# Optimization experiments

Hardware: AMD Instinct MI355X
Metric: run time of the kernel (lower is better)

The kernel has to match this reference:

```python
import jax, jax.numpy as jnp
from jax import lax
import numpy as np

# Model hyperparameters (match init_kwargs)
NUM_STEPS = 6
N_ETYPES = 8
D_IN = 128
D_OUT = 128
B, N, E = 32, 1024, 262144  # graphs, nodes per graph, total edges


def setup_inputs() -> dict:
    key = jax.random.key(0)
    ks = jax.random.split(key, 24)
    s = 0.05  # param scale for numeric stability over 6 GRU steps
    inp = {
        "h": jax.random.normal(ks[0], (B, N, D_IN), jnp.float32),
        "src": jax.random.randint(ks[1], (E,), 0, B * N, jnp.int32),
        "dst": jax.random.randint(ks[2], (E,), 0, B * N, jnp.int32),
        "etype": jax.random.randint(ks[3], (E,), 0, N_ETYPES, jnp.int32),
        "W_msg": jax.random.normal(ks[4], (N_ETYPES, D_OUT, D_OUT), jnp.float32) * s,
        "b_msg": jax.random.normal(ks[5], (N_ETYPES, D_OUT), jnp.float32) * s,
        "w_ih": jax.random.normal(ks[6], (3 * D_OUT, D_OUT), jnp.float32) * s,
        "w_hh": jax.random.normal(ks[7], (3 * D_OUT, D_OUT), jnp.float32) * s,
        "b_ih": jax.random.normal(ks[8], (3 * D_OUT,), jnp.float32) * s,
        "b_hh": jax.random.normal(ks[9], (3 * D_OUT,), jnp.float32) * s,
        "conv1_w": jax.random.normal(ks[10], (D_OUT, D_OUT, 3), jnp.float32) * s,
        "conv1_b": jax.random.normal(ks[11], (D_OUT,), jnp.float32) * s,
        "conv2_w": jax.random.normal(ks[12], (D_OUT, D_OUT, 1), jnp.float32) * s,
        "conv2_b": jax.random.normal(ks[13], (D_OUT,), jnp.float32) * s,
        "cc1_w": jax.random.normal(ks[14], (D_IN + D_OUT, D_IN + D_OUT, 3), jnp.float32) * s,
        "cc1_b": jax.random.normal(ks[15], (D_IN + D_OUT,), jnp.float32) * s,
        "cc2_w": jax.random.normal(ks[16], (D_IN + D_OUT, D_IN + D_OUT, 1), jnp.float32) * s,
        "cc2_b": jax.random.normal(ks[17], (D_IN + D_OUT,), jnp.float32) * s,
        "mlp_y_w": jax.random.normal(ks[18], (1, D_OUT), jnp.float32) * s,
        "mlp_y_b": jax.random.normal(ks[19], (1,), jnp.float32) * s,
        "mlp_z_w": jax.random.normal(ks[20], (1, D_IN + D_OUT), jnp.float32) * s,
        "mlp_z_b": jax.random.normal(ks[21], (1,), jnp.float32) * s,
    }
    return inp


def _conv1d(x, w, b):
    # x: [B, C_in, L], w: [C_out, C_in, K]
    y = lax.conv_general_dilated(x, w, (1,), "VALID",
                                 dimension_numbers=("NCW", "OIW", "NCW"))
    return y + b[None, :, None]


def _maxpool1d(x, k, stride):
    return lax.reduce_window(x, -jnp.inf, lax.max,
                             (1, 1, k), (1, 1, stride), "VALID")


def _ggnn(h0, src, dst, etype, W_msg, b_msg, w_ih, w_hh, b_ih, b_hh):
    # h0: [BN, D_OUT] (in_feats == out_feats so no zero-padding needed)
    n_nodes = h0.shape[0]

    def step(h, _):
        # transform each node by every etype weight: [BN, T, O]
        t = jnp.einsum("nd,tod->nto", h, W_msg) + b_msg
        m = t[src, etype]                                   # [E, O] gather
        a = jax.ops.segment_sum(m, dst, num_segments=n_nodes)  # scatter-add
        # torch.nn.GRUCell(a, h)
        gi = a @ w_ih.T + b_ih
        gh = h @ w_hh.T + b_hh
        i_r, i_z, i_n = jnp.split(gi, 3, axis=-1)
        h_r, h_z, h_n = jnp.split(gh, 3, axis=-1)
        r = jax.nn.sigmoid(i_r + h_r)
        z = jax.nn.sigmoid(i_z + h_z)
        n = jnp.tanh(i_n + r * h_n)
        return (1.0 - z) * n + z * h, None

    h_final, _ = lax.scan(step, h0, None, length=NUM_STEPS)
    return h_final


def reference(h, src, dst, etype, W_msg, b_msg, w_ih, w_hh, b_ih, b_hh,
              conv1_w, conv1_b, conv2_w, conv2_b, cc1_w, cc1_b, cc2_w, cc2_b,
              mlp_y_w, mlp_y_b, mlp_z_w, mlp_z_b):
    b, n, d = h.shape
    x = h.reshape(b * n, d)
    h_next = _ggnn(x, src, dst, etype, W_msg, b_msg, w_ih, w_hh, b_ih, b_hh)
    h_i = h_next.reshape(b, n, -1)                   # [B, N, O]
    c_i = jnp.concatenate([h_i, h], axis=-1)          # [B, N, O+D]

    Y_1 = _maxpool1d(jax.nn.relu(_conv1d(h_i.transpose(0, 2, 1), conv1_w, conv1_b)), 3, 2)
    Y_2 = _maxpool1d(jax.nn.relu(_conv1d(Y_1, conv2_w, conv2_b)), 2, 2).transpose(0, 2, 1)
    Z_1 = _maxpool1d(jax.nn.relu(_conv1d(c_i.transpose(0, 2, 1), cc1_w, cc1_b)), 3, 2)
    Z_2 = _maxpool1d(jax.nn.relu(_conv1d(Z_1, cc2_w, cc2_b)), 2, 2).transpose(0, 2, 1)

    before_avg = (Y_2 @ mlp_y_w.T + mlp_y_b) * (Z_2 @ mlp_z_w.T + mlp_z_b)  # [B, L, 1]
    avg = before_avg.mean(axis=1)                     # [B, 1]
    return jax.nn.sigmoid(avg).squeeze(-1)            # [B]
```

## Files before the change

### kernel.cpp

```cpp
#include <hip/hip_runtime.h>
#include <math.h>

#define BB 32
#define NNODE 1024
#define BN 32768
#define NE 262144
#define DD 128
#define NT 8
#define NSTEPS 6
#define NBIN 16
#define SORT_CAP (NE + 2048)
#define NTILES_F 2064
#define M_CAP (NE + 2048)

typedef __attribute__((ext_vector_type(8))) short bf16x8;
typedef __attribute__((ext_vector_type(4))) float f32x4;

static __device__ __forceinline__ float4 ld4(const float* p) { return *(const float4*)p; }
static __device__ __forceinline__ float sigmoidf_(float x) { return 1.f / (1.f + expf(-x)); }
static __device__ __forceinline__ unsigned f2b(float f) {
    unsigned u = __float_as_uint(f);
    return (u + 0x7FFFu + ((u >> 16) & 1u)) >> 16;
}
static __device__ __forceinline__ float b2f(unsigned short b) {
    return __uint_as_float(((unsigned)b) << 16);
}
static __device__ __forceinline__ unsigned pk(float a, float b) {
    return f2b(a) | (f2b(b) << 16);
}
static __device__ __forceinline__ unsigned bmax2(unsigned a, unsigned b) {
    unsigned ah = a & 0xFFFF0000u, bh = b & 0xFFFF0000u;
    unsigned al = a & 0x0000FFFFu, bl = b & 0x0000FFFFu;
    return (ah > bh ? ah : bh) | (al > bl ? al : bl);
}
static __device__ __forceinline__ uint4 bmax4(uint4 a, uint4 b) {
    return make_uint4(bmax2(a.x, b.x), bmax2(a.y, b.y), bmax2(a.z, b.z), bmax2(a.w, b.w));
}

static constexpr size_t OFF_HCUR = 0;
static constexpr size_t OFF_HBF  = OFF_HCUR + (size_t)BN * DD * 4;
static constexpr size_t OFF_CNT  = OFF_HBF  + (size_t)BN * DD * 2;
static constexpr size_t OFF_DOFF = OFF_CNT  + (size_t)BN * NT * 4;
static constexpr size_t OFF_DBLK = OFF_DOFF + (size_t)BN * 4;
static constexpr size_t OFF_HB   = OFF_DBLK + 512;
static constexpr size_t OFF_SSRC = OFF_HB   + 256;
static constexpr size_t OFF_SDST = OFF_SSRC + (size_t)SORT_CAP * 4;
static constexpr size_t OFF_SQ   = OFF_SDST + (size_t)SORT_CAP * 4;
static constexpr size_t OFF_DCUR = OFF_SQ   + (size_t)SORT_CAP * 4;
static constexpr size_t OFF_DEG  = OFF_DCUR + (size_t)BN * 4;
static constexpr size_t OFF_WMB  = OFF_DEG  + (size_t)BN * 4;
static constexpr size_t OFF_WIHB = OFF_WMB  + (size_t)NT * DD * DD * 2;
static constexpr size_t OFF_WHHB = OFF_WIHB + (size_t)3 * DD * DD * 2;
static constexpr size_t OFF_W1PY = OFF_WHHB + (size_t)3 * DD * DD * 2;
static constexpr size_t OFF_W1PZ = OFF_W1PY + (size_t)3 * 128 * 128 * 2;
static constexpr size_t OFF_W2YB = OFF_W1PZ + (size_t)3 * 256 * 256 * 2;
static constexpr size_t OFF_W2ZB = OFF_W2YB + (size_t)128 * 128 * 2;
static constexpr size_t OFF_ABF  = OFF_W2ZB + (size_t)256 * 256 * 2;
static constexpr size_t OFF_H0BF = OFF_ABF  + (size_t)BN * DD * 2;
static constexpr size_t OFF_UN   = OFF_H0BF + (size_t)BN * DD * 2;
static constexpr size_t OFF_M    = OFF_UN;
static constexpr size_t OFF_U1Y  = OFF_UN;
static constexpr size_t OFF_U1Z  = OFF_U1Y + (size_t)32 * 1024 * 128 * 2;
static constexpr size_t OFF_QY   = OFF_U1Z + (size_t)32 * 1024 * 256 * 2;
static constexpr size_t OFF_QZ   = OFF_QY  + (size_t)32 * 255 * 128 * 4;
static constexpr size_t CONV_SZ  = (size_t)32 * 1024 * 128 * 2 + (size_t)32 * 1024 * 256 * 2
                                 + (size_t)32 * 255 * 128 * 4 + (size_t)32 * 255 * 256 * 4;
static constexpr size_t M_SZ     = (size_t)M_CAP * 128 * 2;
static constexpr size_t UN_SZ    = (M_SZ > CONV_SZ ? M_SZ : CONV_SZ);
static constexpr size_t WS_NEED  = OFF_UN + UN_SZ;

#define PREP_BLOCKS 6133
__global__ void k_prep(const float* __restrict__ h_in, float* __restrict__ hcur,
                       unsigned short* __restrict__ hbf, unsigned short* __restrict__ h0bf,
                       const float* __restrict__ Wmsg, unsigned short* __restrict__ wmb,
                       const float* __restrict__ wih, unsigned short* __restrict__ wihb,
                       const float* __restrict__ whh, unsigned short* __restrict__ whhb,
                       const float* __restrict__ c2w, unsigned short* __restrict__ w2yb,
                       const float* __restrict__ z2w, unsigned short* __restrict__ w2zb,
                       const float* __restrict__ c1w, unsigned short* __restrict__ w1py,
                       const float* __restrict__ z1w, unsigned short* __restrict__ w1pz,
                       int* __restrict__ cnt, int* __restrict__ hb,
                       int* __restrict__ ssrc, int* __restrict__ sdst)
{
    int blk = blockIdx.x, tid = threadIdx.x;
    if (blk < 4096) {
        int i = blk * 256 + tid;
        float4 v = ((const float4*)h_in)[i];
        ((float4*)hcur)[i] = v;
        uint2 p = make_uint2(pk(v.x, v.y), pk(v.z, v.w));
        ((uint2*)hbf)[i] = p;
        ((uint2*)h0bf)[i] = p;
    } else if (blk < 4224) {
        int i = (blk - 4096) * 256 + tid;
        float4 v = ((const float4*)Wmsg)[i];
        ((uint2*)wmb)[i] = make_uint2(pk(v.x, v.y), pk(v.z, v.w));
    } else if (blk < 4272) {
        int i = (blk - 4224) * 256 + tid;
        float4 v = ((const float4*)wih)[i];
        ((uint2*)wihb)[i] = make_uint2(pk(v.x, v.y), pk(v.z, v.w));
    } else if (blk < 4320) {
        int i = (blk - 4272) * 256 + tid;
        float4 v = ((const float4*)whh)[i];
        ((uint2*)whhb)[i] = make_uint2(pk(v.x, v.y), pk(v.z, v.w));
    } else if (blk < 4336) {
        int i = (blk - 4320) * 256 + tid;
        float4 v = ((const float4*)c2w)[i];
        ((uint2*)w2yb)[i] = make_uint2(pk(v.x, v.y), pk(v.z, v.w));
    } else if (blk < 4400) {
        int i = (blk - 4336) * 256 + tid;
        float4 v = ((const float4*)z2w)[i];
        ((uint2*)w2zb)[i] = make_uint2(pk(v.x, v.y), pk(v.z, v.w));
    } else if (blk < 4592) {
        int g = (blk - 4400) * 256 + tid;
        int k = g >> 14, rem = g & 16383;
        w1py[g] = (unsigned short)f2b(c1w[(size_t)rem * 3 + k]);
    } else if (blk < 5360) {
        int g = (blk - 4592) * 256 + tid;
        int k = g >> 16, rem = g & 65535;
        w1pz[g] = (unsigned short)f2b(z1w[(size_t)rem * 3 + k]);
    } else if (blk < 5616) {
        ((uint4*)cnt)[(blk - 5360) * 256 + tid] = make_uint4(0, 0, 0, 0);
    } else if (blk < 5617) {
        if (tid < 64) hb[tid] = 0;
    } else if (blk < 5875) {
        ((uint4*)ssrc)[(blk - 5617) * 256 + tid] = make_uint4(0, 0, 0, 0);
    } else {
        ((uint4*)sdst)[(blk - 5875) * 256 + tid] = make_uint4(~0u, ~0u, ~0u, ~0u);
    }
}


__global__ void k_hist(const int* __restrict__ et, const int* __restrict__ dst,
                       int* __restrict__ hb, int* __restrict__ cnt)
{
    __shared__ int lh[NBIN];
    int tid = threadIdx.x;
    if (tid < NBIN) lh[tid] = 0;
    __syncthreads();
    int base = blockIdx.x * 1024;
    for (int k = 0; k < 4; ++k) {
        int e = base + tid + k * 256;
        int t = et[e], d = dst[e];
        atomicAdd(&lh[((d >> 14) << 3) | t], 1);
        atomicAdd(&cnt[d * NT + t], 1);
    }
    __syncthreads();
    if (tid < NBIN) atomicAdd(&hb[tid], lh[tid]);
}

__global__ void k_degA(const int* __restrict__ cnt, int* __restrict__ deg,
                       int* __restrict__ doff, int* __restrict__ dblk)
{
    __shared__ int ps[256];
    int tid = threadIdx.x;
    int v = blockIdx.x * 256 + tid;
    const int* cv = cnt + (size_t)v * NT;
    int d = 0;
#pragma unroll
    for (int t = 0; t < NT; ++t) d += cv[t];
    deg[v] = d;
    ps[tid] = d;
    __syncthreads();
    for (int off = 1; off < 256; off <<= 1) {
        int x = 0;
        if (tid >= off) x = ps[tid - off];
        __syncthreads();
        ps[tid] += x;
        __syncthreads();
    }
    doff[v] = ps[tid] - d;
    if (tid == 255) dblk[blockIdx.x] = ps[255];
}

__global__ void k_scan2(int* __restrict__ hb, int* __restrict__ dblk)
{
    __shared__ int s[128];
    int tid = threadIdx.x;
    s[tid] = dblk[tid];
    __syncthreads();
    if (tid == 0) {
        int acc = 0;
        for (int t = 0; t < NBIN; ++t) {
            hb[16 + t] = acc;
            hb[33 + t] = acc;
            acc += ((hb[t] + 127) >> 7) << 7;
        }
        hb[32] = acc;
        int run = 0;
        for (int i = 0; i < 128; ++i) {
            int x = s[i]; s[i] = run; run += x;
        }
    }
    __syncthreads();
    dblk[tid] = s[tid];
}

__global__ void k_degB(int* __restrict__ doff, int* __restrict__ dcur,
                       const int* __restrict__ dblk)
{
    int v = blockIdx.x * 256 + threadIdx.x;
    int o = doff[v] + dblk[blockIdx.x];
    doff[v] = o;
    dcur[v] = o;
}

__global__ void k_scatter(const int* __restrict__ src, const int* __restrict__ dst,
                          const int* __restrict__ et, int* __restrict__ hb,
                          int* __restrict__ dcur,
                          int* __restrict__ ssrc, int* __restrict__ sdst, int* __restrict__ sq)
{
    __shared__ int lc[NBIN], lbase[NBIN];
    int tid = threadIdx.x;
    if (tid < NBIN) lc[tid] = 0;
    __syncthreads();
    int base = blockIdx.x * 1024;
    int myk[4], myr[4];
    for (int k = 0; k < 4; ++k) {
        int e = base + tid * 4 + k;
        int kk = ((dst[e] >> 14) << 3) | et[e];
        myk[k] = kk;
        myr[k] = atomicAdd(&lc[kk], 1);
    }
    __syncthreads();
    if (tid < NBIN) lbase[tid] = atomicAdd(&hb[33 + tid], lc[tid]);
    __syncthreads();
    for (int k = 0; k < 4; ++k) {
        int e = base + tid * 4 + k;
        int p = lbase[myk[k]] + myr[k];
        int d = dst[e];
        ssrc[p] = src[e];
        sdst[p] = d;
        sq[p] = atomicAdd(&dcur[d], 1);
    }
}


__launch_bounds__(256, 4)
__global__ void k_msg(const int* __restrict__ ssrc, const int* __restrict__ sdst,
                      const int* __restrict__ sq, const int* __restrict__ hb,
                      const unsigned short* __restrict__ hbf,
                      const unsigned short* __restrict__ wmb,
                      unsigned short* __restrict__ m)
{
    __shared__ __align__(16) unsigned short As[128 * 64];
    __shared__ __align__(16) unsigned short Ws[128 * 64];
    __shared__ int sdl[128], ssl[128], sql[128];
    int base = blockIdx.x * 128;
    if (base >= hb[32]) return;
    int bin = 0;
#pragma unroll
    for (int i = 1; i < NBIN; ++i) if (base >= hb[16 + i]) bin = i;
    int t = bin & 7;
    int tid = threadIdx.x;
    if (tid < 128) { sdl[tid] = sdst[base + tid]; ssl[tid] = ssrc[base + tid]; sql[tid] = sq[base + tid]; }
    __syncthreads();
    int lane = tid & 63, wvv = tid >> 6;
    int wm = (wvv >> 1) * 64, wn = (wvv & 1) * 64;
    int lr = lane & 15, lk = lane >> 4;
    f32x4 acc[4][4];
#pragma unroll
    for (int i = 0; i < 4; ++i)
#pragma unroll
        for (int j = 0; j < 4; ++j) acc[i][j] = (f32x4){0.f, 0.f, 0.f, 0.f};

    int r = tid >> 1, halfc = tid & 1;
    unsigned boff = r * 128 + halfc * 64;
    unsigned sw = (r & 7) << 4;
    for (int c0 = 0; c0 < DD; c0 += 64) {
        if (c0) __syncthreads();
        {
            const uint4* hp = (const uint4*)(hbf + (size_t)ssl[r] * DD + c0 + halfc * 32);
            const uint4* wp = (const uint4*)(wmb + (size_t)t * DD * DD + (size_t)r * DD + c0 + halfc * 32);
#pragma unroll
            for (int c = 0; c < 4; ++c) {
                unsigned byte = (boff + c * 16) ^ sw;
                *(uint4*)((char*)As + byte) = hp[c];
                *(uint4*)((char*)Ws + byte) = wp[c];
            }
        }
        __syncthreads();
#pragma unroll
        for (int kc = 0; kc < 2; ++kc) {
            int cb = kc * 64 + lk * 16;
            bf16x8 af[4], bfv[4];
#pragma unroll
            for (int mi = 0; mi < 4; ++mi) {
                int row = wm + mi * 16 + lr;
                af[mi] = *(const bf16x8*)((const char*)As + ((row * 128 + cb) ^ ((row & 7) << 4)));
            }
#pragma unroll
            for (int ni = 0; ni < 4; ++ni) {
                int row = wn + ni * 16 + lr;
                bfv[ni] = *(const bf16x8*)((const char*)Ws + ((row * 128 + cb) ^ ((row & 7) << 4)));
            }
#pragma unroll
            for (int mi = 0; mi < 4; ++mi)
#pragma unroll
                for (int ni = 0; ni < 4; ++ni)
                    acc[mi][ni] = __builtin_amdgcn_mfma_f32_16x16x32_bf16(af[mi], bfv[ni], acc[mi][ni], 0, 0, 0);
        }
    }
    __syncthreads();
    {
        unsigned short* tgt = wn ? Ws : As;
#pragma unroll
        for (int mi = 0; mi < 4; ++mi)
#pragma unroll
            for (int ni = 0; ni < 4; ++ni)
#pragma unroll
                for (int rg = 0; rg < 4; ++rg) {
                    int er = wm + mi * 16 + lk * 4 + rg;
                    int col = (wn + ni * 16 + lr) & 63;
                    unsigned byte = ((unsigned)(er * 128 + col * 2)) ^ ((er & 7) << 4);
                    *(unsigned short*)((char*)tgt + byte) = (unsigned short)f2b(acc[mi][ni][rg]);
                }
    }
    __syncthreads();
    int orow = tid >> 4, ochunk = tid & 15;
#pragma unroll
    for (int p = 0; p < 8; ++p) {
        int row = p * 16 + orow;
        if (sdl[row] >= 0) {
            const char* srcb = (ochunk < 8) ? (const char*)As : (const char*)Ws;
            unsigned byte = ((unsigned)(row * 128 + (ochunk & 7) * 16)) ^ ((row & 7) << 4);
            uint4 v = *(const uint4*)(srcb + byte);
            *(uint4*)(m + (size_t)sql[row] * 128 + ochunk * 8) = v;
        }
    }
}


__launch_bounds__(256)
__global__ void k_agg(const unsigned short* __restrict__ m, const int* __restrict__ deg,
                      const int* __restrict__ doff, const int* __restrict__ cnt,
                      const float* __restrict__ bmsg, unsigned short* __restrict__ abf)
{
    __shared__ float bm[NT * DD];
    int tid = threadIdx.x;
    *(float4*)&bm[tid * 4] = ld4(bmsg + tid * 4);
    __syncthreads();
    int wv = tid >> 6, lane = tid & 63;
    int v = blockIdx.x * 4 + wv;
    int lh = lane >> 5;
    int lc = lane & 31;
    float a0 = 0.f, a1 = 0.f, a2 = 0.f, a3 = 0.f;
    if (lh == 0) {
        const int* cv = cnt + (size_t)v * NT;
        int c0 = lc * 4;
#pragma unroll
        for (int t = 0; t < NT; ++t) {
            float c = (float)cv[t];
            a0 += c * bm[t * DD + c0];
            a1 += c * bm[t * DD + c0 + 1];
            a2 += c * bm[t * DD + c0 + 2];
            a3 += c * bm[t * DD + c0 + 3];
        }
    }
    int d = deg[v], off = doff[v];
    const uint2* mr = (const uint2*)m;
    int npair = d >> 1;
    for (int i = 0; i < npair; ++i) {
        uint2 w = mr[(size_t)(off + 2 * i + lh) * 32 + lc];
        a0 += b2f((unsigned short)(w.x & 0xFFFF));
        a1 += b2f((unsigned short)(w.x >> 16));
        a2 += b2f((unsigned short)(w.y & 0xFFFF));
        a3 += b2f((unsigned short)(w.y >> 16));
    }
    if ((d & 1) && lh == 0) {
        uint2 w = mr[(size_t)(off + d - 1) * 32 + lc];
        a0 += b2f((unsigned short)(w.x & 0xFFFF));
        a1 += b2f((unsigned short)(w.x >> 16));
        a2 += b2f((unsigned short)(w.y & 0xFFFF));
        a3 += b2f((unsigned short)(w.y >> 16));
    }
    a0 += __shfl_xor(a0, 32);
    a1 += __shfl_xor(a1, 32);
    a2 += __shfl_xor(a2, 32);
    a3 += __shfl_xor(a3, 32);
    if (lh == 0)
        ((uint2*)abf)[(size_t)v * 32 + lc] = make_uint2(pk(a0, a1), pk(a2, a3));
}


__launch_bounds__(512, 2)
__global__ void k_gru(const unsigned short* __restrict__ abf, float* __restrict__ h,
                      unsigned short* __restrict__ hbf,
                      const unsigned short* __restrict__ wihb, const unsigned short* __restrict__ whhb,
                      const float* __restrict__ bih, const float* __restrict__ bhh)
{
    __shared__ __align__(16) unsigned short Xs[128 * 128];
    __shared__ __align__(16) unsigned short Ws2[128 * 128];
    int m0 = blockIdx.x * 128;
    int tid = threadIdx.x;
    int lane = tid & 63, wv = tid >> 6;
    int wm = (wv >> 1) * 32, wn = (wv & 1) * 64;
    int lr = lane & 15, lk = lane >> 4;
    f32x4 aR[2][4], aZ[2][4], aI[2][4], aH[2][4];
#pragma unroll
    for (int i = 0; i < 2; ++i)
#pragma unroll
        for (int j = 0; j < 4; ++j) {
            aR[i][j] = (f32x4){0.f, 0.f, 0.f, 0.f};
            aZ[i][j] = (f32x4){0.f, 0.f, 0.f, 0.f};
            aI[i][j] = (f32x4){0.f, 0.f, 0.f, 0.f};
            aH[i][j] = (f32x4){0.f, 0.f, 0.f, 0.f};
        }
    int rx = tid >> 2, qx = tid & 3;
    unsigned bx = rx * 256 + qx * 64, swx = (rx & 7) << 4;
#pragma unroll
    for (int pass = 0; pass < 2; ++pass) {
        const unsigned short* X = pass ? hbf : abf;
        const unsigned short* W = pass ? whhb : wihb;
#pragma unroll
        for (int g = 0; g < 3; ++g) {
            __syncthreads();
            if (g == 0) {
                const uint4* sp = (const uint4*)(X + (size_t)(m0 + rx) * DD + qx * 32);
#pragma unroll
                for (int c = 0; c < 4; ++c)
                    *(uint4*)((char*)Xs + ((bx + c * 16) ^ swx)) = sp[c];
            }
            {
                const uint4* wp = (const uint4*)(W + (size_t)(g * DD + rx) * DD + qx * 32);
#pragma unroll
                for (int c = 0; c < 4; ++c)
                    *(uint4*)((char*)Ws2 + ((bx + c * 16) ^ swx)) = wp[c];
            }
            __syncthreads();
#pragma unroll
            for (int kc = 0; kc < 4; ++kc) {
                int cb = kc * 64 + lk * 16;
                bf16x8 af[2], bfv[4];
#pragma unroll
                for (int mi = 0; mi < 2; ++mi) {
                    int row = wm + mi * 16 + lr;
                    af[mi] = *(const bf16x8*)((const char*)Xs + ((row * 256 + cb) ^ ((row & 7) << 4)));
                }
#pragma unroll
                for (int ni = 0; ni < 4; ++ni) {
                    int row = wn + ni * 16 + lr;
                    bfv[ni] = *(const bf16x8*)((const char*)Ws2 + ((row * 256 + cb) ^ ((row & 7) << 4)));
                }
#pragma unroll
                for (int mi = 0; mi < 2; ++mi)
#pragma unroll
                    for (int ni = 0; ni < 4; ++ni) {
                        if (g == 0)
                            aR[mi][ni] = __builtin_amdgcn_mfma_f32_16x16x32_bf16(af[mi], bfv[ni], aR[mi][ni], 0, 0, 0);
                        else if (g == 1)
                            aZ[mi][ni] = __builtin_amdgcn_mfma_f32_16x16x32_bf16(af[mi], bfv[ni], aZ[mi][ni], 0, 0, 0);
                        else if (pass == 0)
                            aI[mi][ni] = __builtin_amdgcn_mfma_f32_16x16x32_bf16(af[mi], bfv[ni], aI[mi][ni], 0, 0, 0);
                        else
                            aH[mi][ni] = __builtin_amdgcn_mfma_f32_16x16x32_bf16(af[mi], bfv[ni], aH[mi][ni], 0, 0, 0);
                    }
            }
        }
    }
#pragma unroll
    for (int ni = 0; ni < 4; ++ni) {
        int col = wn + ni * 16 + lr;
        float br_ = bih[col] + bhh[col];
        float bz_ = bih[DD + col] + bhh[DD + col];
        float bin_ = bih[2 * DD + col], bhn_ = bhh[2 * DD + col];
#pragma unroll
        for (int mi = 0; mi < 2; ++mi)
#pragma unroll
            for (int rg = 0; rg < 4; ++rg) {
                int v = m0 + wm + mi * 16 + lk * 4 + rg;
                float rr = sigmoidf_(aR[mi][ni][rg] + br_);
                float zz = sigmoidf_(aZ[mi][ni][rg] + bz_);
                float nn = tanhf(aI[mi][ni][rg] + bin_ + rr * (aH[mi][ni][rg] + bhn_));
                float hold = h[(size_t)v * DD + col];
                float hnew = (1.f - zz) * nn + zz * hold;
                h[(size_t)v * DD + col] = hnew;
                hbf[(size_t)v * DD + col] = (unsigned short)f2b(hnew);
            }
    }
}


template <int CIN>
__launch_bounds__(256, 2)
__global__ void k_conv1m(const unsigned short* __restrict__ hbf, const unsigned short* __restrict__ h0bf,
                         const unsigned short* __restrict__ w1p, const float* __restrict__ bias,
                         unsigned short* __restrict__ U1)
{
    __shared__ __align__(16) unsigned short As[128 * 64];
    __shared__ __align__(16) unsigned short Ws[128 * 64];
    int p0 = blockIdx.x * 128, b = blockIdx.y, n0 = blockIdx.z * 128;
    int tid = threadIdx.x;
    int lane = tid & 63, wv = tid >> 6;
    int wm = (wv >> 1) * 64, wn = (wv & 1) * 64;
    int lr = lane & 15, lk = lane >> 4;
    f32x4 acc[4][4];
#pragma unroll
    for (int i = 0; i < 4; ++i)
#pragma unroll
        for (int j = 0; j < 4; ++j) acc[i][j] = (f32x4){0.f, 0.f, 0.f, 0.f};

    int r = tid >> 1, halfc = tid & 1;
    unsigned boff = r * 128 + halfc * 64;
    unsigned sw = (r & 7) << 4;
#pragma unroll
    for (int k = 0; k < 3; ++k) {
        for (int c0 = 0; c0 < CIN; c0 += 64) {
            __syncthreads();
            {
                int row = p0 + k + r; if (row > NNODE - 1) row = NNODE - 1;
                int ci = c0 + halfc * 32;
                const unsigned short* srcp = (CIN == 128 || ci < 128)
                    ? hbf  + ((size_t)(b * NNODE + row)) * DD + ci
                    : h0bf + ((size_t)(b * NNODE + row)) * DD + (ci - 128);
                const uint4* sp = (const uint4*)srcp;
#pragma unroll
                for (int c = 0; c < 4; ++c)
                    *(uint4*)((char*)As + ((boff + c * 16) ^ sw)) = sp[c];
            }
            {
                const uint4* wp = (const uint4*)(w1p + ((size_t)k * CIN + n0 + r) * CIN + c0 + halfc * 32);
#pragma unroll
                for (int c = 0; c < 4; ++c)
                    *(uint4*)((char*)Ws + ((boff + c * 16) ^ sw)) = wp[c];
            }
            __syncthreads();
#pragma unroll
            for (int kc = 0; kc < 2; ++kc) {
                int cb = kc * 64 + lk * 16;
                bf16x8 af[4], bfv[4];
#pragma unroll
                for (int mi = 0; mi < 4; ++mi) {
                    int row = wm + mi * 16 + lr;
                    af[mi] = *(const bf16x8*)((const char*)As + ((row * 128 + cb) ^ ((row & 7) << 4)));
                }
#pragma unroll
                for (int ni = 0; ni < 4; ++ni) {
                    int row = wn + ni * 16 + lr;
                    bfv[ni] = *(const bf16x8*)((const char*)Ws + ((row * 128 + cb) ^ ((row & 7) << 4)));
                }
#pragma unroll
                for (int mi = 0; mi < 4; ++mi)
#pragma unroll
                    for (int ni = 0; ni < 4; ++ni)
                        acc[mi][ni] = __builtin_amdgcn_mfma_f32_16x16x32_bf16(af[mi], bfv[ni], acc[mi][ni], 0, 0, 0);
            }
        }
    }
#pragma unroll
    for (int ni = 0; ni < 4; ++ni) {
        int co = n0 + wn + ni * 16 + lr;
        float bs = bias[co];
#pragma unroll
        for (int mi = 0; mi < 4; ++mi)
#pragma unroll
            for (int rg = 0; rg < 4; ++rg) {
                int pos = p0 + wm + mi * 16 + lk * 4 + rg;
                if (pos < NNODE - 2) {
                    float v = fmaxf(0.f, acc[mi][ni][rg] + bs);
                    U1[((size_t)b * NNODE + pos) * CIN + co] = (unsigned short)f2b(v);
                }
            }
    }
}


template <int CIN>
__launch_bounds__(256, 2)
__global__ void k_conv2m(const unsigned short* __restrict__ U1, const unsigned short* __restrict__ w2b,
                         const float* __restrict__ bias, float* __restrict__ Q)
{
    __shared__ __align__(16) unsigned short As[128 * 64];
    __shared__ __align__(16) unsigned short Ws[128 * 64];
    int m0 = blockIdx.x * 128, b = blockIdx.y, n0 = blockIdx.z * 128;
    int tid = threadIdx.x;
    int lane = tid & 63, wv = tid >> 6;
    int wm = (wv >> 1) * 64, wn = (wv & 1) * 64;
    int lr = lane & 15, lk = lane >> 4;
    f32x4 acc[4][4];
#pragma unroll
    for (int i = 0; i < 4; ++i)
#pragma unroll
        for (int j = 0; j < 4; ++j) acc[i][j] = (f32x4){0.f, 0.f, 0.f, 0.f};

    int r = tid >> 1, halfc = tid & 1;
    unsigned boff = r * 128 + halfc * 64;
    unsigned sw = (r & 7) << 4;
    for (int c0 = 0; c0 < CIN; c0 += 64) {
        __syncthreads();
        {
            int pr = 2 * (m0 + r);
            int r0 = pr, r1 = pr + 1, r2v = pr + 2;
            if (r2v > NNODE - 1) r2v = NNODE - 1;
            if (r1 > NNODE - 1) r1 = NNODE - 1;
            int ci = c0 + halfc * 32;
            const unsigned short* bp = U1 + (size_t)b * NNODE * CIN + ci;
            const uint4* p0q = (const uint4*)(bp + (size_t)r0 * CIN);
            const uint4* p1q = (const uint4*)(bp + (size_t)r1 * CIN);
            const uint4* p2q = (const uint4*)(bp + (size_t)r2v * CIN);
#pragma unroll
            for (int c = 0; c < 4; ++c) {
                uint4 mm = bmax4(bmax4(p0q[c], p1q[c]), p2q[c]);
                *(uint4*)((char*)As + ((boff + c * 16) ^ sw)) = mm;
            }
        }
        {
            const uint4* wp = (const uint4*)(w2b + (size_t)(n0 + r) * CIN + c0 + halfc * 32);
#pragma unroll
            for (int c = 0; c < 4; ++c)
                *(uint4*)((char*)Ws + ((boff + c * 16) ^ sw)) = wp[c];
        }
        __syncthreads();
#pragma unroll
        for (int kc = 0; kc < 2; ++kc) {
            int cb = kc * 64 + lk * 16;
            bf16x8 af[4], bfv[4];
#pragma unroll
            for (int mi = 0; mi < 4; ++mi) {
                int row = wm + mi * 16 + lr;
                af[mi] = *(const bf16x8*)((const char*)As + ((row * 128 + cb) ^ ((row & 7) << 4)));
            }
#pragma unroll
            for (int ni = 0; ni < 4; ++ni) {
                int row = wn + ni * 16 + lr;
                bfv[ni] = *(const bf16x8*)((const char*)Ws + ((row * 128 + cb) ^ ((row & 7) << 4)));
            }
#pragma unroll
            for (int mi = 0; mi < 4; ++mi)
#pragma unroll
                for (int ni = 0; ni < 4; ++ni)
                    acc[mi][ni] = __builtin_amdgcn_mfma_f32_16x16x32_bf16(af[mi], bfv[ni], acc[mi][ni], 0, 0, 0);
        }
    }
#pragma unroll
    for (int ni = 0; ni < 4; ++ni) {
        int co = n0 + wn + ni * 16 + lr;
        float bs = bias[co];
#pragma unroll
        for (int mi = 0; mi < 4; ++mi) {
            int l0 = m0 + wm + mi * 16 + lk * 4;
            float v0 = fmaxf(0.f, acc[mi][ni][0] + bs);
            float v1 = fmaxf(0.f, acc[mi][ni][1] + bs);
            float v2 = fmaxf(0.f, acc[mi][ni][2] + bs);
            float v3 = fmaxf(0.f, acc[mi][ni][3] + bs);
            int jq = l0 >> 1;
            if (jq < 255)     Q[((size_t)b * 255 + jq) * CIN + co]     = fmaxf(v0, v1);
            if (jq + 1 < 255) Q[((size_t)b * 255 + jq + 1) * CIN + co] = fmaxf(v2, v3);
        }
    }
}


__launch_bounds__(256)
__global__ void k_final(const float* __restrict__ QY, const float* __restrict__ QZ,
                        const float* __restrict__ wy, const float* __restrict__ by,
                        const float* __restrict__ wz, const float* __restrict__ bz,
                        float* __restrict__ out)
{
    int b = blockIdx.x, tid = threadIdx.x;
    float p = 0.f;
    if (tid < 255) {
        const float* qy = QY + ((size_t)(b * 255 + tid)) * 128;
        const float* qz = QZ + ((size_t)(b * 255 + tid)) * 256;
        float dy = 0.f, dz = 0.f;
        for (int c = 0; c < 128; c += 4) {
            float4 q = ld4(qy + c), wv = ld4(wy + c);
            dy += q.x * wv.x + q.y * wv.y + q.z * wv.z + q.w * wv.w;
        }
        for (int c = 0; c < 256; c += 4) {
            float4 q = ld4(qz + c), wv = ld4(wz + c);
            dz += q.x * wv.x + q.y * wv.y + q.z * wv.z + q.w * wv.w;
        }
        p = (dy + by[0]) * (dz + bz[0]);
    }
    __shared__ float red[4];
    for (int off = 32; off > 0; off >>= 1) p += __shfl_down(p, off);
    if ((tid & 63) == 0) red[tid >> 6] = p;
    __syncthreads();
    if (tid == 0) {
        float s = red[0] + red[1] + red[2] + red[3];
        out[b] = 1.f / (1.f + expf(-s / 255.f));
    }
}


extern "C" void kernel_launch(void* const* d_in, const int* in_sizes, int n_in,
                              void* d_out, int out_size, void* d_ws, size_t ws_size,
                              hipStream_t stream)
{
    const float* h_in = (const float*)d_in[0];
    const int* src = (const int*)d_in[1];
    const int* dst = (const int*)d_in[2];
    const int* et  = (const int*)d_in[3];
    const float* Wmsg = (const float*)d_in[4];
    const float* bmsg = (const float*)d_in[5];
    const float* wih = (const float*)d_in[6];
    const float* whh = (const float*)d_in[7];
    const float* bih = (const float*)d_in[8];
    const float* bhh = (const float*)d_in[9];
    const float* c1w = (const float*)d_in[10];
    const float* c1b = (const float*)d_in[11];
    const float* c2w = (const float*)d_in[12];
    const float* c2b = (const float*)d_in[13];
    const float* z1w = (const float*)d_in[14];
    const float* z1b = (const float*)d_in[15];
    const float* z2w = (const float*)d_in[16];
    const float* z2b = (const float*)d_in[17];
    const float* wy  = (const float*)d_in[18];
    const float* by  = (const float*)d_in[19];
    const float* wz  = (const float*)d_in[20];
    const float* bz  = (const float*)d_in[21];
    float* out = (float*)d_out;

    if (ws_size < WS_NEED) return;

    char* ws = (char*)d_ws;
    float* hcur = (float*)(ws + OFF_HCUR);
    unsigned short* hbf  = (unsigned short*)(ws + OFF_HBF);
    int*   cnt  = (int*)(ws + OFF_CNT);
    int*   doff = (int*)(ws + OFF_DOFF);
    int*   dblk = (int*)(ws + OFF_DBLK);
    int*   hb   = (int*)(ws + OFF_HB);
    int*   ssrc = (int*)(ws + OFF_SSRC);
    int*   sdst = (int*)(ws + OFF_SDST);
    int*   sq   = (int*)(ws + OFF_SQ);
    int*   dcur = (int*)(ws + OFF_DCUR);
    int*   deg  = (int*)(ws + OFF_DEG);
    unsigned short* wmb  = (unsigned short*)(ws + OFF_WMB);
    unsigned short* wihb = (unsigned short*)(ws + OFF_WIHB);
    unsigned short* whhb = (unsigned short*)(ws + OFF_WHHB);
    unsigned short* w1py = (unsigned short*)(ws + OFF_W1PY);
    unsigned short* w1pz = (unsigned short*)(ws + OFF_W1PZ);
    unsigned short* w2yb = (unsigned short*)(ws + OFF_W2YB);
    unsigned short* w2zb = (unsigned short*)(ws + OFF_W2ZB);
    unsigned short* abf  = (unsigned short*)(ws + OFF_ABF);
    unsigned short* h0bf = (unsigned short*)(ws + OFF_H0BF);
    unsigned short* mbuf = (unsigned short*)(ws + OFF_M);
    unsigned short* U1Y  = (unsigned short*)(ws + OFF_U1Y);
    unsigned short* U1Z  = (unsigned short*)(ws + OFF_U1Z);
    float* QY   = (float*)(ws + OFF_QY);
    float* QZ   = (float*)(ws + OFF_QZ);

    k_prep<<<PREP_BLOCKS, 256, 0, stream>>>(h_in, hcur, hbf, h0bf, Wmsg, wmb, wih, wihb, whh, whhb,
                                            c2w, w2yb, z2w, w2zb, c1w, w1py, z1w, w1pz,
                                            cnt, hb, ssrc, sdst);

    k_hist<<<256, 256, 0, stream>>>(et, dst, hb, cnt);
    k_degA<<<128, 256, 0, stream>>>(cnt, deg, doff, dblk);
    k_scan2<<<1, 128, 0, stream>>>(hb, dblk);
    k_degB<<<128, 256, 0, stream>>>(doff, dcur, dblk);
    k_scatter<<<256, 256, 0, stream>>>(src, dst, et, hb, dcur, ssrc, sdst, sq);

    for (int s = 0; s < NSTEPS; ++s) {
        k_msg<<<NTILES_F, 256, 0, stream>>>(ssrc, sdst, sq, hb, hbf, wmb, mbuf);
        k_agg<<<BN / 4, 256, 0, stream>>>(mbuf, deg, doff, cnt, bmsg, abf);
        k_gru<<<BN / 128, 512, 0, stream>>>(abf, hcur, hbf, wihb, whhb, bih, bhh);
    }

    k_conv1m<128><<<dim3(8, 32, 1), 256, 0, stream>>>(hbf, h0bf, w1py, c1b, U1Y);
    k_conv2m<128><<<dim3(4, 32, 1), 256, 0, stream>>>(U1Y, w2yb, c2b, QY);
    k_conv1m<256><<<dim3(8, 32, 2), 256, 0, stream>>>(hbf, h0bf, w1pz, z1b, U1Z);
    k_conv2m<256><<<dim3(4, 32, 2), 256, 0, stream>>>(U1Z, w2zb, z2b, QZ);
    k_final<<<32, 256, 0, stream>>>(QY, QZ, wy, by, wz, bz, out);
}
```

Baseline: 554.0 us.

## Reuse shifted activation tile across conv taps in conv1 kernel

The k=3 conv1 kernel now loads one activation tile with 136 rows per channel chunk and reads it at row offsets for each of the three taps, instead of reloading the input tile once per tap. All three tap weight tiles are staged in LDS together, so there are fewer barriers and global loads. LDS use grows to about 66KB, which may lower occupancy. Separately, conv2 launch bounds are raised to request 4 blocks per SM, which may cause register spills.

```diff
diff --git a/kernel.cpp b/kernel.cpp
--- a/kernel.cpp
+++ b/kernel.cpp
@@ -486,8 +486,8 @@
                          const unsigned short* __restrict__ w1p, const float* __restrict__ bias,
                          unsigned short* __restrict__ U1)
 {
-    __shared__ __align__(16) unsigned short As[128 * 64];
-    __shared__ __align__(16) unsigned short Ws[128 * 64];
+    __shared__ __align__(16) unsigned short Ae[136 * 64];
+    __shared__ __align__(16) unsigned short Ws3[3][128 * 64];
     int p0 = blockIdx.x * 128, b = blockIdx.y, n0 = blockIdx.z * 128;
     int tid = threadIdx.x;
     int lane = tid & 63, wv = tid >> 6;
@@ -502,41 +502,55 @@
     int r = tid >> 1, halfc = tid & 1;
     unsigned boff = r * 128 + halfc * 64;
     unsigned sw = (r & 7) << 4;
-#pragma unroll
-    for (int k = 0; k < 3; ++k) {
-        for (int c0 = 0; c0 < CIN; c0 += 64) {
-            __syncthreads();
-            {
-                int row = p0 + k + r; if (row > NNODE - 1) row = NNODE - 1;
-                int ci = c0 + halfc * 32;
-                const unsigned short* srcp = (CIN == 128 || ci < 128)
-                    ? hbf  + ((size_t)(b * NNODE + row)) * DD + ci
-                    : h0bf + ((size_t)(b * NNODE + row)) * DD + (ci - 128);
-                const uint4* sp = (const uint4*)srcp;
-#pragma unroll
-                for (int c = 0; c < 4; ++c)
-                    *(uint4*)((char*)As + ((boff + c * 16) ^ sw)) = sp[c];
-            }
-            {
-                const uint4* wp = (const uint4*)(w1p + ((size_t)k * CIN + n0 + r) * CIN + c0 + halfc * 32);
-#pragma unroll
-                for (int c = 0; c < 4; ++c)
-                    *(uint4*)((char*)Ws + ((boff + c * 16) ^ sw)) = wp[c];
-            }
-            __syncthreads();
+    for (int c0 = 0; c0 < CIN; c0 += 64) {
+        __syncthreads();
+        {
+            int row = p0 + r; if (row > NNODE - 1) row = NNODE - 1;
+            int ci = c0 + halfc * 32;
+            const unsigned short* srcp = (CIN == 128 || ci < 128)
+                ? hbf  + ((size_t)(b * NNODE + row)) * DD + ci
+                : h0bf + ((size_t)(b * NNODE + row)) * DD + (ci - 128);
+            const uint4* sp = (const uint4*)srcp;
+#pragma unroll
+            for (int c = 0; c < 4; ++c)
+                *(uint4*)((char*)Ae + ((boff + c * 16) ^ sw)) = sp[c];
+        }
+        if (tid < 4) {
+            int rr = 128 + (tid >> 1), hh = tid & 1;
+            int row = p0 + rr; if (row > NNODE - 1) row = NNODE - 1;
+            int ci = c0 + hh * 32;
+            const unsigned short* srcp = (CIN == 128 || ci < 128)
+                ? hbf  + ((size_t)(b * NNODE + row)) * DD + ci
+                : h0bf + ((size_t)(b * NNODE + row)) * DD + (ci - 128);
+            const uint4* sp = (const uint4*)srcp;
+            unsigned bo = rr * 128 + hh * 64, sw2 = (rr & 7) << 4;
+#pragma unroll
+            for (int c = 0; c < 4; ++c)
+                *(uint4*)((char*)Ae + ((bo + c * 16) ^ sw2)) = sp[c];
+        }
+#pragma unroll
+        for (int k = 0; k < 3; ++k) {
+            const uint4* wp = (const uint4*)(w1p + ((size_t)k * CIN + n0 + r) * CIN + c0 + halfc * 32);
+#pragma unroll
+            for (int c = 0; c < 4; ++c)
+                *(uint4*)((char*)Ws3[k] + ((boff + c * 16) ^ sw)) = wp[c];
+        }
+        __syncthreads();
+#pragma unroll
+        for (int k = 0; k < 3; ++k) {
 #pragma unroll
             for (int kc = 0; kc < 2; ++kc) {
                 int cb = kc * 64 + lk * 16;
                 bf16x8 af[4], bfv[4];
 #pragma unroll
                 for (int mi = 0; mi < 4; ++mi) {
-                    int row = wm + mi * 16 + lr;
-                    af[mi] = *(const bf16x8*)((const char*)As + ((row * 128 + cb) ^ ((row & 7) << 4)));
+                    int rowA = wm + mi * 16 + lr + k;
+                    af[mi] = *(const bf16x8*)((const char*)Ae + ((rowA * 128 + cb) ^ ((rowA & 7) << 4)));
                 }
 #pragma unroll
                 for (int ni = 0; ni < 4; ++ni) {
                     int row = wn + ni * 16 + lr;
-                    bfv[ni] = *(const bf16x8*)((const char*)Ws + ((row * 128 + cb) ^ ((row & 7) << 4)));
+                    bfv[ni] = *(const bf16x8*)((const char*)Ws3[k] + ((row * 128 + cb) ^ ((row & 7) << 4)));
                 }
 #pragma unroll
                 for (int mi = 0; mi < 4; ++mi)
@@ -565,7 +579,7 @@
 
 
 template <int CIN>
-__launch_bounds__(256, 2)
+__launch_bounds__(256, 4)
 __global__ void k_conv2m(const unsigned short* __restrict__ U1, const unsigned short* __restrict__ w2b,
                          const float* __restrict__ bias, float* __restrict__ Q)
 {
```

New measurement: 556.5 us. Within noise of the previous version (+0.4%).
